# Optimization experiments

Measured on AMD Instinct MI355X. Metric: run time of the kernel, lower is better.

The kernel has to match this reference:

```python
import jax, jax.numpy as jnp
import numpy as np

B, DIM, MID, H, W = 4, 256, 128, 128, 128
EPS = 1e-5


def _conv(x, w, pad):
    # x: [B,C,H,W], w: [O,I,k,k]
    return jax.lax.conv_general_dilated(
        x, w, window_strides=(1, 1), padding=[(pad, pad), (pad, pad)],
        dimension_numbers=('NCHW', 'OIHW', 'NCHW'))


def _bn(x, g, b, m, v):
    inv = jax.lax.rsqrt(v + EPS)
    scale = (g * inv)[None, :, None, None]
    shift = (b - m * g * inv)[None, :, None, None]
    return x * scale + shift


def _convbnrelu(x, w, g, b, m, v):
    return jax.nn.relu(_bn(_conv(x, w, 1), g, b, m, v))


# CornerNet directional pools: sequential max-accumulation scans.
def top_pool(x):     # max over y' >= y  -> reversed cummax along H
    return jax.lax.cummax(x, axis=2, reverse=True)

def bottom_pool(x):  # max over y' <= y
    return jax.lax.cummax(x, axis=2)

def left_pool(x):    # max over x' >= x
    return jax.lax.cummax(x, axis=3, reverse=True)

def right_pool(x):   # max over x' <= x
    return jax.lax.cummax(x, axis=3)


def setup_inputs() -> dict:
    key = jax.random.key(0)
    ks = jax.random.split(key, 32)
    it = iter(ks)

    def w(shape, scale=0.05):
        return jax.random.normal(next(it), shape, jnp.float32) * scale

    def bn_params(c):
        return (jnp.ones((c,), jnp.float32) + 0.1 * jax.random.normal(next(it), (c,), jnp.float32),
                0.1 * jax.random.normal(next(it), (c,), jnp.float32),
                0.1 * jax.random.normal(next(it), (c,), jnp.float32),
                jax.random.uniform(next(it), (c,), jnp.float32) + 0.5)

    inp = {'x': jax.random.normal(next(it), (B, DIM, H, W), jnp.float32)}

    inp['p1_w'] = w((MID, DIM, 3, 3))
    inp['p1_g'], inp['p1_b'], inp['p1_m'], inp['p1_v'] = bn_params(MID)
    inp['p2_w'] = w((MID, DIM, 3, 3))
    inp['p2_g'], inp['p2_b'], inp['p2_m'], inp['p2_v'] = bn_params(MID)
    inp['p_w'] = w((DIM, MID, 3, 3))
    inp['p_g'], inp['p_b'], inp['p_m'], inp['p_v'] = bn_params(DIM)
    inp['c1_w'] = w((DIM, DIM, 1, 1))
    inp['c1_g'], inp['c1_b'], inp['c1_m'], inp['c1_v'] = bn_params(DIM)
    inp['c2_w'] = w((DIM, DIM, 3, 3))
    inp['c2_g'], inp['c2_b'], inp['c2_m'], inp['c2_v'] = bn_params(DIM)
    return inp


def reference(x,
              p1_w, p1_g, p1_b, p1_m, p1_v,
              p2_w, p2_g, p2_b, p2_m, p2_v,
              p_w, p_g, p_b, p_m, p_v,
              c1_w, c1_g, c1_b, c1_m, c1_v,
              c2_w, c2_g, c2_b, c2_m, c2_v):
    # branch 1: conv-bn-relu -> top pool -> bottom pool
    pool1 = bottom_pool(top_pool(_convbnrelu(x, p1_w, p1_g, p1_b, p1_m, p1_v)))
    # branch 2: conv-bn-relu -> left pool -> right pool
    pool2 = right_pool(left_pool(_convbnrelu(x, p2_w, p2_g, p2_b, p2_m, p2_v)))
    # merge branch
    p_bn1 = _bn(_conv(pool1 + pool2, p_w, 1), p_g, p_b, p_m, p_v)
    # skip branch: 1x1 conv + bn
    bn1 = _bn(_conv(x, c1_w, 0), c1_g, c1_b, c1_m, c1_v)
    # residual add + relu, then final conv-bn-relu
    return _convbnrelu(jax.nn.relu(p_bn1 + bn1), c2_w, c2_g, c2_b, c2_m, c2_v)
```

## Files before the change

kernel.cpp:

```cpp
#include <hip/hip_runtime.h>
#include <hip/hip_bf16.h>
#include <math.h>


constexpr int NB   = 4;
constexpr int CDIM = 256;
constexpr int CMID = 128;
constexpr int HS   = 128;
constexpr int WS   = 128;
constexpr float EPS = 1e-5f;

typedef __bf16 bf16x8 __attribute__((ext_vector_type(8)));
typedef float  f32x4  __attribute__((ext_vector_type(4)));

#define AS1 __attribute__((address_space(1)))
#define AS3 __attribute__((address_space(3)))

__device__ __forceinline__ void load16_lds(const void* gsrc, void* ldst) {
    __builtin_amdgcn_global_load_lds((const AS1 unsigned int*)gsrc,
                                     (AS3 unsigned int*)ldst, 16, 0, 0);
}

__global__ __launch_bounds__(512) void k_prep(
    const float* __restrict__ xin, __hip_bfloat16* __restrict__ Xc,
    const float* __restrict__ p1w, const float* __restrict__ p2w,
    const float* __restrict__ c2w, const float* __restrict__ c1w,
    __hip_bfloat16* __restrict__ Aw1, __hip_bfloat16* __restrict__ Aw2,
    __hip_bfloat16* __restrict__ Aw5, __hip_bfloat16* __restrict__ Aw4,
    f32x4* __restrict__ zdst)
{
    __shared__ __hip_bfloat16 lds[128 * 264];
    const int bid = blockIdx.x;
    const int t   = threadIdx.x;

    if (bid < 512) {
        const int y = bid >> 2;
        const int b = bid & 3;
#pragma unroll
        for (int k = 0; k < 16; ++k) {
            int idx = t + k * 512;
            int ci = idx >> 5, x4 = idx & 31;
            f32x4 v = *(const f32x4*)(xin + (((size_t)b * CDIM + ci) * HS + y) * WS + x4 * 4);
#pragma unroll
            for (int j = 0; j < 4; ++j)
                lds[(x4 * 4 + j) * 264 + ci] = __float2bfloat16(v[j]);
        }
        __syncthreads();
#pragma unroll
        for (int k = 0; k < 8; ++k) {
            int i = t + k * 512;
            int x = i >> 5, c8 = i & 31;
            bf16x8 vv = *(const bf16x8*)(lds + x * 264 + c8 * 8);
            *(bf16x8*)(Xc + ((size_t)(b * 128 + y) * 128 + x) * 256 + c8 * 8) = vv;
        }
        return;
    }

    const int u  = (bid - 512) * 2 + (t >> 8);
    const int tl = t & 255;
    if (u < 512) {
        const float* W; __hip_bfloat16* A; int co;
        if (u < 128)      { W = p1w; A = Aw1; co = u; }
        else if (u < 256) { W = p2w; A = Aw2; co = u - 128; }
        else              { W = c2w; A = Aw5; co = u - 256; }
#pragma unroll
        for (int tap = 0; tap < 9; ++tap)
            A[(size_t)co * 2304 + tap * 256 + tl] =
                __float2bfloat16(W[((size_t)co * CDIM + tl) * 9 + tap]);
    } else if (u < 640) {
        int base = (u - 512) * 512 + tl;
        Aw4[base]       = __float2bfloat16(c1w[base]);
        Aw4[base + 256] = __float2bfloat16(c1w[base + 256]);
    } else if (u < 768) {
        zdst[(size_t)(u - 640) * 256 + tl] = (f32x4){0.f, 0.f, 0.f, 0.f};
    } else if (u == 768) {
        if (tl < 16) zdst[32768 + tl] = (f32x4){0.f, 0.f, 0.f, 0.f};
    }
}

template<int MODE>
__global__ __launch_bounds__(256, 2) void k_conv3(
    const __hip_bfloat16* __restrict__ Xc,
    const __hip_bfloat16* __restrict__ AwA, const __hip_bfloat16* __restrict__ AwB,
    const float* __restrict__ zbuf,
    const float* __restrict__ g1, const float* __restrict__ b1,
    const float* __restrict__ m1, const float* __restrict__ v1,
    const float* __restrict__ g2, const float* __restrict__ b2,
    const float* __restrict__ m2, const float* __restrict__ v2,
    float* __restrict__ out0, unsigned* __restrict__ cmax,
    unsigned* __restrict__ rmax, int CO)
{
    const int y0     = blockIdx.x * 2;
    const int branch = blockIdx.y;
    const int b      = blockIdx.z;
    const int co0    = (MODE == 0) ? branch * 128 : 0;

    const __hip_bfloat16* Aw = (MODE == 1 && branch) ? AwB : AwA;
    const float* gg  = (MODE == 1 && branch) ? g2 : g1;
    const float* bbp = (MODE == 1 && branch) ? b2 : b1;
    const float* mmp = (MODE == 1 && branch) ? m2 : m1;
    const float* vvp = (MODE == 1 && branch) ? v2 : v1;

    __shared__ __hip_bfloat16 smem[644 * 32];
    __shared__ float s_sc[128], s_sh[128];
    __shared__ unsigned s_red[2][128];
    char* smb = (char*)smem;

    const int t    = threadIdx.x;
    const int lane = t & 63;
    const int w    = t >> 6;
    const int ml   = lane & 15;
    const int q    = lane >> 4;
    const int mbase = (w >> 1) * 64;
    const int nbase = (w & 1) * 64;

    if (t < 128) {
        int co = co0 + t;
        float iv = rsqrtf(vvp[co] + EPS);
        float sc = gg[co] * iv;
        s_sc[t] = sc;
        s_sh[t] = bbp[co] - mmp[co] * sc;
        if (MODE == 1) { s_red[0][t] = 0u; s_red[1][t] = 0u; }
    }

    f32x4 acc[2][4][4];
#pragma unroll
    for (int yy = 0; yy < 2; ++yy)
#pragma unroll
        for (int mt = 0; mt < 4; ++mt)
#pragma unroll
            for (int nt = 0; nt < 4; ++nt)
                acc[yy][mt][nt] = (f32x4){0.f, 0.f, 0.f, 0.f};

    const __hip_bfloat16* bbase = Xc + (size_t)(b * 128) * 128 * 256;

#pragma unroll 1
    for (int ky = 0; ky < 3; ++ky) {
        const int yd0 = y0 + ky - 1;
        const __hip_bfloat16* arow = Aw + (size_t)co0 * 2304 + (3 * ky) * 256;
#pragma unroll 1
        for (int cih = 0; cih < 8; ++cih) {
            const int cb = cih * 32;
#pragma unroll
            for (int p = 0; p < 11; ++p) {
                int i = t + p * 256;
                if (i < 2576) {
                    int row = i >> 2, sl = i & 3;
                    int c = sl ^ ((row >> 1) & 3);
                    const __hip_bfloat16* src;
                    if (row < 384) {
                        int j = row >> 7, col = row & 127;
                        src = arow + (size_t)col * 2304 + j * 256 + cb + c * 8;
                    } else {
                        int rbi = row - 384;
                        int yy  = rbi >= 130;
                        int xi  = rbi - 130 * yy;
                        int gy  = yd0 + yy, gx = xi - 1;
                        src = ((unsigned)gy < 128u && (unsigned)gx < 128u)
                            ? bbase + ((size_t)(gy * 128 + gx)) * 256 + cb + c * 8
                            : (const __hip_bfloat16*)((const char*)zbuf + c * 16);
                    }
                    load16_lds(src, smb + (size_t)i * 16);
                }
            }
            __syncthreads();
#pragma unroll
            for (int j = 0; j < 3; ++j) {
                bf16x8 af[4];
#pragma unroll
                for (int mt = 0; mt < 4; ++mt) {
                    const int ra = j * 128 + mbase + mt * 16 + ml;
                    const int sa = q ^ ((ra >> 1) & 3);
                    af[mt] = *(const bf16x8*)(smb + (size_t)ra * 64 + sa * 16);
                }
#pragma unroll
                for (int yy = 0; yy < 2; ++yy) {
                    bf16x8 bfv[4];
#pragma unroll
                    for (int nt = 0; nt < 4; ++nt) {
                        const int rb = 384 + yy * 130 + nbase + nt * 16 + ml + j;
                        const int sb = q ^ ((rb >> 1) & 3);
                        bfv[nt] = *(const bf16x8*)(smb + (size_t)rb * 64 + sb * 16);
                    }
#pragma unroll
                    for (int mt = 0; mt < 4; ++mt)
#pragma unroll
                        for (int nt = 0; nt < 4; ++nt)
                            acc[yy][mt][nt] = __builtin_amdgcn_mfma_f32_16x16x32_bf16(
                                af[mt], bfv[nt], acc[yy][mt][nt], 0, 0, 0);
                }
            }
            __syncthreads();
        }
    }

#pragma unroll
    for (int mt = 0; mt < 4; ++mt) {
#pragma unroll
        for (int r = 0; r < 4; ++r) {
            const int col = mbase + mt * 16 + q * 4 + r;
            const float sc = s_sc[col], sh = s_sh[col];
            const int co = co0 + col;
            unsigned rmx0 = 0u, rmx1 = 0u;
#pragma unroll
            for (int nt = 0; nt < 4; ++nt) {
                float va = fmaxf(acc[0][mt][nt][r] * sc + sh, 0.f);
                float vb = fmaxf(acc[1][mt][nt][r] * sc + sh, 0.f);
                const int x = nbase + nt * 16 + ml;
                if (MODE == 0) {
                    __builtin_nontemporal_store(va,
                        out0 + (((size_t)b * CO + co) * HS + y0)     * WS + x);
                    __builtin_nontemporal_store(vb,
                        out0 + (((size_t)b * CO + co) * HS + y0 + 1) * WS + x);
                } else if (branch == 0) {
                    atomicMax(cmax + ((size_t)(b * 128 + co)) * 128 + x,
                              __float_as_uint(fmaxf(va, vb)));
                } else {
                    rmx0 = max(rmx0, __float_as_uint(va));
                    rmx1 = max(rmx1, __float_as_uint(vb));
                }
            }
            if (MODE == 1 && branch == 1) {
                atomicMax(&s_red[0][col], rmx0);
                atomicMax(&s_red[1][col], rmx1);
            }
        }
    }
    if (MODE == 1 && branch == 1) {
        __syncthreads();
        if (t < 128) {
            atomicMax(rmax + ((size_t)(b * 128 + t)) * 128 + y0,     s_red[0][t]);
            atomicMax(rmax + ((size_t)(b * 128 + t)) * 128 + y0 + 1, s_red[1][t]);
        }
    }
}

__global__ __launch_bounds__(128) void k_uv(
    const float* __restrict__ pw, const float* __restrict__ cm,
    const float* __restrict__ rm,
    __hip_bfloat16* __restrict__ U, __hip_bfloat16* __restrict__ V)
{
    const int co   = blockIdx.x;
    const int b    = blockIdx.y;
    const int mode = blockIdx.z;
    const int p    = threadIdx.x;
    float acc0 = 0.f, acc1 = 0.f, acc2 = 0.f;
    const float* base = (mode == 0) ? cm : rm;
    for (int ci = 0; ci < CMID; ++ci) {
        const float* w9 = pw + (co * CMID + ci) * 9;
        float s0[3], s1[3], s2[3];
        if (mode == 0) {
#pragma unroll
            for (int k = 0; k < 3; ++k) {
                float a = w9[k], qq = w9[3 + k], r = w9[6 + k];
                s0[k] = qq + r; s1[k] = a + qq + r; s2[k] = a + qq;
            }
        } else {
#pragma unroll
            for (int k = 0; k < 3; ++k) {
                float a = w9[k*3 + 0], qq = w9[k*3 + 1], r = w9[k*3 + 2];
                s0[k] = qq + r; s1[k] = a + qq + r; s2[k] = a + qq;
            }
        }
        const float* v = base + (b * CMID + ci) * 128;
#pragma unroll
        for (int k = 0; k < 3; ++k) {
            int pos = p + k - 1;
            if ((unsigned)pos < 128u) {
                float vv = v[pos];
                acc0 += s0[k] * vv; acc1 += s1[k] * vv; acc2 += s2[k] * vv;
            }
        }
    }
    __hip_bfloat16* dst = (mode == 0) ? U : V;
    dst[((0 * NB + b) * CDIM + co) * 128 + p] = __float2bfloat16(acc0);
    dst[((1 * NB + b) * CDIM + co) * 128 + p] = __float2bfloat16(acc1);
    dst[((2 * NB + b) * CDIM + co) * 128 + p] = __float2bfloat16(acc2);
}

__global__ __launch_bounds__(256, 2) void k_merge_mfma(
    const __hip_bfloat16* __restrict__ Xc, const __hip_bfloat16* __restrict__ Aw4,
    const __hip_bfloat16* __restrict__ U, const __hip_bfloat16* __restrict__ V,
    const float* __restrict__ pg, const float* __restrict__ pb,
    const float* __restrict__ pm, const float* __restrict__ pv,
    const float* __restrict__ cg, const float* __restrict__ cb,
    const float* __restrict__ cmn, const float* __restrict__ cv,
    __hip_bfloat16* __restrict__ Rc)
{
    const int y = blockIdx.x;
    const int b = blockIdx.y;
    __shared__ __hip_bfloat16 smem[32768];
    __shared__ float s_psc[256], s_psh[256], s_csc[256], s_csh[256];
    __shared__ float s_v0[256], s_vm[256], s_v1[256];
    char* smb = (char*)smem;
    const int t = threadIdx.x, lane = t & 63, w = t >> 6;
    const int ml = lane & 15, q = lane >> 4;
    const int mbase = w * 64;
    const int yc = (y == 0) ? 0 : ((y == HS - 1) ? 2 : 1);

    {
        int co = t;
        float iv = rsqrtf(pv[co] + EPS);
        float psc = pg[co] * iv;
        s_psc[co] = psc;
        s_psh[co] = pb[co] - pm[co] * psc;
        float iv2 = rsqrtf(cv[co] + EPS);
        float csc = cg[co] * iv2;
        s_csc[co] = csc;
        s_csh[co] = cb[co] - cmn[co] * csc;
        const size_t vb = ((size_t)b * CDIM + co) * 128 + y;
        const size_t cstr = (size_t)NB * CDIM * 128;
        s_v0[co] = __bfloat162float(V[vb]);
        s_vm[co] = __bfloat162float(V[cstr + vb]);
        s_v1[co] = __bfloat162float(V[2 * cstr + vb]);
    }

    f32x4 acc[4][8];
#pragma unroll
    for (int mt = 0; mt < 4; ++mt)
#pragma unroll
        for (int nt = 0; nt < 8; ++nt)
            acc[mt][nt] = (f32x4){0.f, 0.f, 0.f, 0.f};

    const __hip_bfloat16* brow = Xc + (size_t)(b * 128 + y) * 128 * 256;
#pragma unroll 1
    for (int ks = 0; ks < 4; ++ks) {
#pragma unroll
        for (int p = 0; p < 12; ++p) {
            int i   = t + p * 256;
            int row = i >> 3, sl = i & 7;
            int c   = sl ^ (row & 7);
            const __hip_bfloat16* src = (row < 256)
                ? Aw4 + (size_t)row * 256 + ks * 64 + c * 8
                : brow + (size_t)(row - 256) * 256 + ks * 64 + c * 8;
            load16_lds(src, smb + (size_t)i * 16);
        }
        __syncthreads();
#pragma unroll
        for (int s = 0; s < 2; ++s) {
            bf16x8 af[4], bfv[8];
#pragma unroll
            for (int mt = 0; mt < 4; ++mt) {
                const int ra = mbase + mt * 16 + ml;
                const int coff = ((s * 4 + q) ^ (ra & 7)) * 16;
                af[mt] = *(const bf16x8*)(smb + (size_t)ra * 128 + coff);
            }
#pragma unroll
            for (int nt = 0; nt < 8; ++nt) {
                const int rb = 256 + nt * 16 + ml;
                const int coff = ((s * 4 + q) ^ (rb & 7)) * 16;
                bfv[nt] = *(const bf16x8*)(smb + (size_t)rb * 128 + coff);
            }
#pragma unroll
            for (int mt = 0; mt < 4; ++mt)
#pragma unroll
                for (int nt = 0; nt < 8; ++nt)
                    acc[mt][nt] = __builtin_amdgcn_mfma_f32_16x16x32_bf16(
                        af[mt], bfv[nt], acc[mt][nt], 0, 0, 0);
        }
        __syncthreads();
    }

    const __hip_bfloat16* Ub = U + ((size_t)(yc * NB + b) * CDIM + mbase) * 128;
#pragma unroll
    for (int k = 0; k < 16; ++k) {
        int i = lane + k * 64;
        load16_lds(Ub + (size_t)i * 8, smb + (size_t)w * 16384 + (size_t)i * 16);
    }
    __syncthreads();
    const __hip_bfloat16* ulds = smem + w * 8192;

#pragma unroll
    for (int mt = 0; mt < 4; ++mt) {
#pragma unroll
        for (int nt = 0; nt < 8; ++nt) {
            const int x = nt * 16 + ml;
            unsigned long long pk = 0;
#pragma unroll
            for (int r = 0; r < 4; ++r) {
                const int cl = mt * 16 + q * 4 + r;
                const int co = mbase + cl;
                float u  = __bfloat162float(ulds[cl * 128 + x]);
                float vt = (x == 0) ? s_v0[co] : ((x == WS - 1) ? s_v1[co] : s_vm[co]);
                float val = fmaxf((u + vt) * s_psc[co] + s_psh[co]
                                  + acc[mt][nt][r] * s_csc[co] + s_csh[co], 0.f);
                __hip_bfloat16 hb = __float2bfloat16(val);
                unsigned short bits;
                __builtin_memcpy(&bits, &hb, 2);
                pk |= (unsigned long long)bits << (16 * r);
            }
            *(unsigned long long*)((char*)Rc +
                ((size_t)((b * 128 + y) * 128 + x) * 256 + mbase + mt * 16 + q * 4) * 2) = pk;
        }
    }
}

extern "C" void kernel_launch(void* const* d_in, const int* in_sizes, int n_in,
                              void* d_out, int out_size, void* d_ws, size_t ws_size,
                              hipStream_t stream)
{
    (void)in_sizes; (void)n_in; (void)out_size; (void)ws_size;
    const float* x    = (const float*)d_in[0];
    const float* p1_w = (const float*)d_in[1];
    const float* p1_g = (const float*)d_in[2];
    const float* p1_b = (const float*)d_in[3];
    const float* p1_m = (const float*)d_in[4];
    const float* p1_v = (const float*)d_in[5];
    const float* p2_w = (const float*)d_in[6];
    const float* p2_g = (const float*)d_in[7];
    const float* p2_b = (const float*)d_in[8];
    const float* p2_m = (const float*)d_in[9];
    const float* p2_v = (const float*)d_in[10];
    const float* p_w  = (const float*)d_in[11];
    const float* p_g  = (const float*)d_in[12];
    const float* p_b  = (const float*)d_in[13];
    const float* p_m  = (const float*)d_in[14];
    const float* p_v  = (const float*)d_in[15];
    const float* c1_w = (const float*)d_in[16];
    const float* c1_g = (const float*)d_in[17];
    const float* c1_b = (const float*)d_in[18];
    const float* c1_m = (const float*)d_in[19];
    const float* c1_v = (const float*)d_in[20];
    const float* c2_w = (const float*)d_in[21];
    const float* c2_g = (const float*)d_in[22];
    const float* c2_b = (const float*)d_in[23];
    const float* c2_m = (const float*)d_in[24];
    const float* c2_v = (const float*)d_in[25];
    float* out = (float*)d_out;
    char* ws = (char*)d_ws;

    __hip_bfloat16* Xc   = (__hip_bfloat16*)ws;
    __hip_bfloat16* Rc   = (__hip_bfloat16*)(ws + 33554432);
    __hip_bfloat16* Ubuf = (__hip_bfloat16*)(ws + 67108864);
    __hip_bfloat16* Vbuf = (__hip_bfloat16*)(ws + 67895296);
    __hip_bfloat16* Aw1  = (__hip_bfloat16*)(ws + 67108864);
    __hip_bfloat16* Aw2  = (__hip_bfloat16*)(ws + 67698688);
    __hip_bfloat16* Aw5  = (__hip_bfloat16*)(ws + 68681728);
    __hip_bfloat16* Aw4  = (__hip_bfloat16*)(ws + 69861376);
    unsigned*       cmaxU = (unsigned*)(ws + 69992448);
    unsigned*       rmaxU = (unsigned*)(ws + 70254592);
    float*          zbuf  = (float*)(ws + 70516736);

    k_prep<<<dim3(897), 512, 0, stream>>>(
        x, Xc, p1_w, p2_w, c2_w, c1_w, Aw1, Aw2, Aw5, Aw4,
        (f32x4*)(ws + 69992448));

    k_conv3<1><<<dim3(64, 2, 4), 256, 0, stream>>>(
        Xc, Aw1, Aw2, zbuf,
        p1_g, p1_b, p1_m, p1_v, p2_g, p2_b, p2_m, p2_v,
        nullptr, cmaxU, rmaxU, CMID);

    k_uv<<<dim3(256, 4, 2), 128, 0, stream>>>(
        p_w, (const float*)cmaxU, (const float*)rmaxU, Ubuf, Vbuf);

    k_merge_mfma<<<dim3(128, 4), 256, 0, stream>>>(
        Xc, Aw4, Ubuf, Vbuf, p_g, p_b, p_m, p_v,
        c1_g, c1_b, c1_m, c1_v, Rc);

    k_conv3<0><<<dim3(64, 2, 4), 256, 0, stream>>>(
        Rc, Aw5, nullptr, zbuf,
        c2_g, c2_b, c2_m, c2_v, nullptr, nullptr, nullptr, nullptr,
        out, nullptr, nullptr, CDIM);
}
```

Before: 394.2 us.

## Recast U/V projection as bf16 MFMA GEMM with prepacked weights and shifted operand

Replaces the scalar fp32 k_uv kernel with a GEMM formulation. The summed tap weights are prepacked into a bf16 A matrix inside k_prep, and a new k_b2 kernel builds a shifted B matrix from the column and row max vectors. A k_uv_mfma kernel then multiplies the two with MFMA instructions. This removes the per-thread scalar loop over channels, at the cost of an extra launch and bf16 rounding of the intermediate sums. The uv GEMM grid is only 24 blocks, so it underfills the GPU.

```diff
diff --git a/kernel.cpp b/kernel.cpp
--- a/kernel.cpp
+++ b/kernel.cpp
@@ -25,8 +25,10 @@
     const float* __restrict__ xin, __hip_bfloat16* __restrict__ Xc,
     const float* __restrict__ p1w, const float* __restrict__ p2w,
     const float* __restrict__ c2w, const float* __restrict__ c1w,
+    const float* __restrict__ pw,
     __hip_bfloat16* __restrict__ Aw1, __hip_bfloat16* __restrict__ Aw2,
     __hip_bfloat16* __restrict__ Aw5, __hip_bfloat16* __restrict__ Aw4,
+    __hip_bfloat16* __restrict__ sA,
     f32x4* __restrict__ zdst)
 {
     __shared__ __hip_bfloat16 lds[128 * 264];
@@ -75,6 +77,28 @@
         zdst[(size_t)(u - 640) * 256 + tl] = (f32x4){0.f, 0.f, 0.f, 0.f};
     } else if (u == 768) {
         if (tl < 16) zdst[32768 + tl] = (f32x4){0.f, 0.f, 0.f, 0.f};
+    } else if (u >= 770 && u < 2306) {
+        const int su  = u - 770;
+        const int m   = su >= 768;
+        const int rem = su - m * 768;
+        const int v   = rem >> 8;
+        const int co  = rem & 255;
+        const float* w9p = pw + ((size_t)co * CMID) * 9;
+#pragma unroll
+        for (int rep = 0; rep < 2; ++rep) {
+            int kk = tl + rep * 256;
+            if (kk < 384) {
+                int ci = kk / 3, k = kk - 3 * (kk / 3);
+                const float* w9 = w9p + (size_t)ci * 9;
+                int i0 = m ? k * 3 + 0 : k;
+                int i1 = m ? k * 3 + 1 : 3 + k;
+                int i2 = m ? k * 3 + 2 : 6 + k;
+                float s = w9[i1];
+                if (v >= 1) s += w9[i0];
+                if (v <= 1) s += w9[i2];
+                sA[((size_t)(m * 3 + v) * 256 + co) * 384 + kk] = __float2bfloat16(s);
+            }
+        }
     }
 }
 
@@ -235,47 +259,105 @@
     }
 }
 
-__global__ __launch_bounds__(128) void k_uv(
-    const float* __restrict__ pw, const float* __restrict__ cm,
-    const float* __restrict__ rm,
+__global__ __launch_bounds__(256) void k_b2(
+    const float* __restrict__ cm, const float* __restrict__ rm,
+    __hip_bfloat16* __restrict__ Bm)
+{
+    const int p0 = blockIdx.x * 16;
+    const int m  = blockIdx.y;
+    const int b  = blockIdx.z;
+    const int tl = threadIdx.x;
+    const float* basep = (m == 0) ? cm : rm;
+#pragma unroll
+    for (int rep = 0; rep < 2; ++rep) {
+        int kk = tl + rep * 256;
+        if (kk < 384) {
+            int ci = kk / 3, k = kk - 3 * (kk / 3);
+            const float* src = basep + ((size_t)b * 128 + ci) * 128;
+            __hip_bfloat16* dst = Bm + ((size_t)(m * 4 + b) * 128) * 384 + kk;
+#pragma unroll
+            for (int pp = 0; pp < 16; ++pp) {
+                int p = p0 + pp;
+                int pos = p + k - 1;
+                float vv = ((unsigned)pos < 128u) ? src[pos] : 0.f;
+                dst[(size_t)p * 384] = __float2bfloat16(vv);
+            }
+        }
+    }
+}
+
+__global__ __launch_bounds__(256, 2) void k_uv_mfma(
+    const __hip_bfloat16* __restrict__ sA, const __hip_bfloat16* __restrict__ Bm,
     __hip_bfloat16* __restrict__ U, __hip_bfloat16* __restrict__ V)
 {
-    const int co   = blockIdx.x;
-    const int b    = blockIdx.y;
-    const int mode = blockIdx.z;
-    const int p    = threadIdx.x;
-    float acc0 = 0.f, acc1 = 0.f, acc2 = 0.f;
-    const float* base = (mode == 0) ? cm : rm;
-    for (int ci = 0; ci < CMID; ++ci) {
-        const float* w9 = pw + (co * CMID + ci) * 9;
-        float s0[3], s1[3], s2[3];
-        if (mode == 0) {
-#pragma unroll
-            for (int k = 0; k < 3; ++k) {
-                float a = w9[k], qq = w9[3 + k], r = w9[6 + k];
-                s0[k] = qq + r; s1[k] = a + qq + r; s2[k] = a + qq;
-            }
-        } else {
-#pragma unroll
-            for (int k = 0; k < 3; ++k) {
-                float a = w9[k*3 + 0], qq = w9[k*3 + 1], r = w9[k*3 + 2];
-                s0[k] = qq + r; s1[k] = a + qq + r; s2[k] = a + qq;
-            }
-        }
-        const float* v = base + (b * CMID + ci) * 128;
-#pragma unroll
-        for (int k = 0; k < 3; ++k) {
-            int pos = p + k - 1;
-            if ((unsigned)pos < 128u) {
-                float vv = v[pos];
-                acc0 += s0[k] * vv; acc1 += s1[k] * vv; acc2 += s2[k] * vv;
-            }
-        }
-    }
-    __hip_bfloat16* dst = (mode == 0) ? U : V;
-    dst[((0 * NB + b) * CDIM + co) * 128 + p] = __float2bfloat16(acc0);
-    dst[((1 * NB + b) * CDIM + co) * 128 + p] = __float2bfloat16(acc1);
-    dst[((2 * NB + b) * CDIM + co) * 128 + p] = __float2bfloat16(acc2);
+    const int v = blockIdx.x;
+    const int b = blockIdx.y;
+    const int m = blockIdx.z;
+    const __hip_bfloat16* A  = sA + (size_t)((m * 3 + v) * 256) * 384;
+    const __hip_bfloat16* Bp = Bm + (size_t)((m * 4 + b) * 128) * 384;
+
+    __shared__ __hip_bfloat16 smem[24576];
+    char* smb = (char*)smem;
+    const int t = threadIdx.x, lane = t & 63, w = t >> 6;
+    const int ml = lane & 15, q = lane >> 4;
+    const int mbase = w * 64;
+
+    f32x4 acc[4][8];
+#pragma unroll
+    for (int mt = 0; mt < 4; ++mt)
+#pragma unroll
+        for (int nt = 0; nt < 8; ++nt)
+            acc[mt][nt] = (f32x4){0.f, 0.f, 0.f, 0.f};
+
+#pragma unroll 1
+    for (int ks = 0; ks < 6; ++ks) {
+#pragma unroll
+        for (int p = 0; p < 12; ++p) {
+            int i   = t + p * 256;
+            int row = i >> 3, sl = i & 7;
+            int c   = sl ^ (row & 7);
+            const __hip_bfloat16* src = (row < 256)
+                ? A  + (size_t)row * 384 + ks * 64 + c * 8
+                : Bp + (size_t)(row - 256) * 384 + ks * 64 + c * 8;
+            load16_lds(src, smb + (size_t)i * 16);
+        }
+        __syncthreads();
+#pragma unroll
+        for (int s = 0; s < 2; ++s) {
+            bf16x8 af[4], bfv[8];
+#pragma unroll
+            for (int mt = 0; mt < 4; ++mt) {
+                const int ra = mbase + mt * 16 + ml;
+                const int coff = ((s * 4 + q) ^ (ra & 7)) * 16;
+                af[mt] = *(const bf16x8*)(smb + (size_t)ra * 128 + coff);
+            }
+#pragma unroll
+            for (int nt = 0; nt < 8; ++nt) {
+                const int rb = 256 + nt * 16 + ml;
+                const int coff = ((s * 4 + q) ^ (rb & 7)) * 16;
+                bfv[nt] = *(const bf16x8*)(smb + (size_t)rb * 128 + coff);
+            }
+#pragma unroll
+            for (int mt = 0; mt < 4; ++mt)
+#pragma unroll
+                for (int nt = 0; nt < 8; ++nt)
+                    acc[mt][nt] = __builtin_amdgcn_mfma_f32_16x16x32_bf16(
+                        af[mt], bfv[nt], acc[mt][nt], 0, 0, 0);
+        }
+        __syncthreads();
+    }
+
+    __hip_bfloat16* dst = ((m == 0) ? U : V) + ((size_t)(v * NB + b) * CDIM) * 128;
+#pragma unroll
+    for (int mt = 0; mt < 4; ++mt)
+#pragma unroll
+        for (int nt = 0; nt < 8; ++nt)
+#pragma unroll
+            for (int r = 0; r < 4; ++r) {
+                const int co = mbase + mt * 16 + q * 4 + r;
+                const int p  = nt * 16 + ml;
+                dst[(size_t)co * 128 + p] = __float2bfloat16(acc[mt][nt][r]);
+            }
 }
 
 __global__ __launch_bounds__(256, 2) void k_merge_mfma(
@@ -431,6 +513,8 @@
 
     __hip_bfloat16* Xc   = (__hip_bfloat16*)ws;
     __hip_bfloat16* Rc   = (__hip_bfloat16*)(ws + 33554432);
+    __hip_bfloat16* sA   = (__hip_bfloat16*)(ws + 33554432);
+    __hip_bfloat16* Bm   = (__hip_bfloat16*)(ws + 34734080);
     __hip_bfloat16* Ubuf = (__hip_bfloat16*)(ws + 67108864);
     __hip_bfloat16* Vbuf = (__hip_bfloat16*)(ws + 67895296);
     __hip_bfloat16* Aw1  = (__hip_bfloat16*)(ws + 67108864);
@@ -441,8 +525,8 @@
     unsigned*       rmaxU = (unsigned*)(ws + 70254592);
     float*          zbuf  = (float*)(ws + 70516736);
 
-    k_prep<<<dim3(897), 512, 0, stream>>>(
-        x, Xc, p1_w, p2_w, c2_w, c1_w, Aw1, Aw2, Aw5, Aw4,
+    k_prep<<<dim3(1665), 512, 0, stream>>>(
+        x, Xc, p1_w, p2_w, c2_w, c1_w, p_w, Aw1, Aw2, Aw5, Aw4, sA,
         (f32x4*)(ws + 69992448));
 
     k_conv3<1><<<dim3(64, 2, 4), 256, 0, stream>>>(
@@ -450,8 +534,9 @@
         p1_g, p1_b, p1_m, p1_v, p2_g, p2_b, p2_m, p2_v,
         nullptr, cmaxU, rmaxU, CMID);
 
-    k_uv<<<dim3(256, 4, 2), 128, 0, stream>>>(
-        p_w, (const float*)cmaxU, (const float*)rmaxU, Ubuf, Vbuf);
+    k_b2<<<dim3(8, 2, 4), 256, 0, stream>>>(
+        (const float*)cmaxU, (const float*)rmaxU, Bm);
+    k_uv_mfma<<<dim3(3, 4, 2), 256, 0, stream>>>(sA, Bm, Ubuf, Vbuf);
 
     k_merge_mfma<<<dim3(128, 4), 256, 0, stream>>>(
         Xc, Aw4, Ubuf, Vbuf, p_g, p_b, p_m, p_v,
```

Result: faster. 348.5 us (-11.6%).
